# Kernel optimization log

Hardware: AMD Instinct MI355X
Metric: run time of the kernel (lower is better)

Reference implementation:

```python
import jax, jax.numpy as jnp
import numpy as np
from math import pi

N = 256        # in_features == out_features
BATCH = 131072


def givens_orthogonal(angles, n):
    """Build an n x n orthogonal matrix as the ordered product of Givens
    rotations G(i, j, theta_k) over pairs i < j in lexicographic order.
    Each rotation mixes rows i and j; applied sequentially via lax.scan."""
    ii, jj = np.triu_indices(n, 1)  # static pair order, len = n*(n-1)//2
    ii = jnp.asarray(ii, dtype=jnp.int32)
    jj = jnp.asarray(jj, dtype=jnp.int32)

    def body(M, t):
        i, j, th = t
        c, s = jnp.cos(th), jnp.sin(th)
        ri, rj = M[i], M[j]
        M = M.at[i].set(c * ri - s * rj)
        M = M.at[j].set(s * ri + c * rj)
        return M, None

    M0 = jnp.eye(n, dtype=angles.dtype)
    M, _ = jax.lax.scan(body, M0, (ii, jj, angles))
    return M


def setup_inputs() -> dict:
    key = jax.random.key(0)
    k1, k2, k3 = jax.random.split(key, 3)
    n_ang = N * (N - 1) // 2  # 32640
    return {
        "x": jax.random.normal(k1, (BATCH, N), dtype=jnp.float32),
        "Uweight": jax.random.uniform(k2, (n_ang,), minval=-pi / 2, maxval=pi / 2, dtype=jnp.float32),
        "Vweight": jax.random.uniform(k3, (n_ang,), minval=-pi / 2, maxval=pi / 2, dtype=jnp.float32),
        "Sweight": jnp.ones((N,), dtype=jnp.float32),
        "bias": jnp.zeros((N,), dtype=jnp.float32),
    }


def reference(x, Uweight, Vweight, Sweight, bias):
    # W = V @ diag(S) @ U^T  (SVD-parametrized weight, out x in)
    # y = x @ W^T + b = ((x @ U) * S) @ V^T + b   (square case in == out)
    U = givens_orthogonal(Uweight, N)  # (in, in) orthogonal
    V = givens_orthogonal(Vweight, N)  # (out, out) orthogonal
    return ((x @ U) * Sweight) @ V.T + bias
```

## Files before the change

### kernel.cpp

```cpp
#include <hip/hip_runtime.h>
#include <hip/hip_bf16.h>
#include <math.h>

#define NN 256
#define NPAIR 32640
#define NSEG 32
#define MAT (NN*NN)

#define MATS0 0
#define MATS1 (MATS0 + 64*MAT)
#define WBT_OFF (MATS1 + 32*MAT)

static __device__ const int BD[NSEG+1] =
    {0,4,8,12,16,20,24,28,32,37,42,47,52,57,62,67,73,79,85,91,97,
     104,111,118,126,134,143,153,164,177,192,213,255};
#define CSL_CAP 1120

typedef __attribute__((ext_vector_type(8))) short short8;
typedef __attribute__((ext_vector_type(4))) float f32x4;

__device__ __forceinline__ short f2bf(float f) {
    __hip_bfloat16 h = __float2bfloat16(f);
    return *reinterpret_cast<short*>(&h);
}

__global__ __launch_bounds__(64) void k_build(const float* __restrict__ au,
                                              const float* __restrict__ av,
                                              float* __restrict__ mats) {
    int b = blockIdx.x;
    int matid = b >> 7;
    int seg   = (b >> 2) & 31;
    int chunk = b & 3;
    int t = threadIdx.x;
    int c0 = chunk * 64;
    int i0 = BD[seg], i1 = BD[seg+1];
    float* outp = mats + (matid * NSEG + seg) * MAT;

    if (c0 + 64 <= i0) {
        for (int id = t; id < 4096; id += 64) {
            int row = id >> 4, c4 = (id & 15) * 4;
            float4 v = {0.f,0.f,0.f,0.f};
            int d = row - (c0 + c4);
            if (d >= 0 && d < 4) ((float*)&v)[d] = 1.0f;
            *(float4*)(outp + row*NN + c0 + c4) = v;
        }
        return;
    }

    __shared__ float M[NN * 64];
    __shared__ float2 csl[CSL_CAP];

    int kbase = 255*i0 - (i0*(i0-1))/2;
    int kend  = 255*i1 - (i1*(i1-1))/2;
    int nrot  = kend - kbase;
    const float* ang = (matid ? av : au) + kbase;
    for (int idx = t; idx < nrot; idx += 64) {
        float s, c;
        sincosf(ang[idx], &s, &c);
        float2 v = {c, s};
        csl[idx] = v;
    }

    int MR = NN - i0;
    for (int rr = 0; rr < MR; ++rr)
        M[rr*64 + t] = (i0 + rr == c0 + t) ? 1.0f : 0.0f;
    __syncthreads();

    for (int i = i0; i < i1; ++i) {
        int jstart = (i + 1 > c0) ? (i + 1) : c0;
        int kl = 255*i - (i*(i-1))/2 + (jstart - i - 1) - kbase;
        float ri = M[(i - i0)*64 + t];
        int j = jstart;
        int ng = (NN - jstart) >> 3;

        float2 cb[8]; float rj[8];
        if (ng > 0) {
#pragma unroll
            for (int u = 0; u < 8; ++u) cb[u] = csl[kl + u];
#pragma unroll
            for (int u = 0; u < 8; ++u) rj[u] = M[(j - i0 + u)*64 + t];
        }
        for (int g = 0; g < ng; ++g) {
            float2 cn[8]; float rn[8];
            if (g + 1 < ng) {
#pragma unroll
                for (int u = 0; u < 8; ++u) cn[u] = csl[kl + 8 + u];
#pragma unroll
                for (int u = 0; u < 8; ++u) rn[u] = M[(j + 8 - i0 + u)*64 + t];
            }
#pragma unroll
            for (int u = 0; u < 8; ++u) {
                float wv = cb[u].y*ri + cb[u].x*rj[u];
                ri       = cb[u].x*ri - cb[u].y*rj[u];
                M[(j - i0 + u)*64 + t] = wv;
            }
#pragma unroll
            for (int u = 0; u < 8; ++u) { cb[u] = cn[u]; rj[u] = rn[u]; }
            j += 8; kl += 8;
        }
        int rem = NN - j;
        if (rem > 0) {
            float2 cc[7]; float r7[7];
#pragma unroll
            for (int u = 0; u < 7; ++u)
                if (u < rem) { cc[u] = csl[kl + u];
                               r7[u] = M[(j - i0 + u)*64 + t]; }
#pragma unroll
            for (int u = 0; u < 7; ++u)
                if (u < rem) {
                    float wv = cc[u].y*ri + cc[u].x*r7[u];
                    ri       = cc[u].x*ri - cc[u].y*r7[u];
                    M[(j - i0 + u)*64 + t] = wv;
                }
        }
        M[(i - i0)*64 + t] = ri;
    }
    __syncthreads();

    for (int id = t; id < 4096; id += 64) {
        int row = id >> 4, c4 = (id & 15) * 4;
        float4 v;
        if (row < i0) {
            v = make_float4(0.f,0.f,0.f,0.f);
            int d = row - (c0 + c4);
            if (d >= 0 && d < 4) ((float*)&v)[d] = 1.0f;
        } else {
            v = *(const float4*)&M[(row - i0)*64 + c4];
        }
        *(float4*)(outp + row*NN + c0 + c4) = v;
    }
}

__global__ __launch_bounds__(256) void k_fold(const float* __restrict__ in,
                                              float* __restrict__ out,
                                              int nOut, int lg, int span) {
    int b = blockIdx.x;
    int np2 = 2 * nOut;
    int m    = b & (np2 - 1);
    int tile = b >> lg;
    int side = (m >= nOut) ? 1 : 0;
    int q = m - side * nOut;
    const float* A = in + (side*np2 + 2*q + 1) * MAT;
    const float* B = in + (side*np2 + 2*q) * MAT;
    float* C = out + m * MAT;
    int i0A = BD[q * span + (span >> 1)];
    int r0 = (tile >> 2) * 64, c0 = (tile & 3) * 64;
    int t = threadIdx.x;

    if (r0 + 64 <= i0A) {
#pragma unroll
        for (int u = 0; u < 4; ++u) {
            int id = u*256 + t;
            int rr = id >> 4, cc = (id & 15) * 4;
            *(float4*)(C + (r0+rr)*NN + c0 + cc) =
                *(const float4*)(B + (r0+rr)*NN + c0 + cc);
        }
        return;
    }

    int kstart = ((r0 < i0A) ? r0 : i0A) & ~31;
    int nt = (NN - kstart) >> 5;

    __shared__ float Ast[2][32][68];
    __shared__ float Bs [2][32][68];
    int tx = t & 15, ty = t >> 4;
    int arow = t >> 3, ak4 = t & 7;
    int bkr = t >> 4, bc4 = t & 15;

    float acc[4][4] = {};
    f32x4 pa0, pa1, pb0, pb1;
    {
        int kt = kstart;
        pa0 = *(const f32x4*)(A + (r0 + arow     )*NN + kt + ak4*4);
        pa1 = *(const f32x4*)(A + (r0 + arow + 32)*NN + kt + ak4*4);
        pb0 = *(const f32x4*)(B + (kt + bkr      )*NN + c0 + bc4*4);
        pb1 = *(const f32x4*)(B + (kt + bkr + 16 )*NN + c0 + bc4*4);
    }
    for (int it = 0; it < nt; ++it) {
        int cur = it & 1;
#pragma unroll
        for (int jj = 0; jj < 4; ++jj) {
            Ast[cur][ak4*4 + jj][arow]      = pa0[jj];
            Ast[cur][ak4*4 + jj][arow + 32] = pa1[jj];
        }
        *(f32x4*)&Bs[cur][bkr     ][bc4*4] = pb0;
        *(f32x4*)&Bs[cur][bkr + 16][bc4*4] = pb1;
        if (it + 1 < nt) {
            int k2 = kstart + (it+1)*32;
            pa0 = *(const f32x4*)(A + (r0 + arow     )*NN + k2 + ak4*4);
            pa1 = *(const f32x4*)(A + (r0 + arow + 32)*NN + k2 + ak4*4);
            pb0 = *(const f32x4*)(B + (k2 + bkr      )*NN + c0 + bc4*4);
            pb1 = *(const f32x4*)(B + (k2 + bkr + 16 )*NN + c0 + bc4*4);
        }
        __syncthreads();
#pragma unroll 8
        for (int kk = 0; kk < 32; ++kk) {
            f32x4 a4 = *(const f32x4*)&Ast[cur][kk][ty*4];
            f32x4 b4 = *(const f32x4*)&Bs [cur][kk][tx*4];
#pragma unroll
            for (int rr = 0; rr < 4; ++rr)
#pragma unroll
                for (int cc = 0; cc < 4; ++cc)
                    acc[rr][cc] = fmaf(a4[rr], b4[cc], acc[rr][cc]);
        }
    }
#pragma unroll
    for (int rr = 0; rr < 4; ++rr) {
        float4 o = {acc[rr][0], acc[rr][1], acc[rr][2], acc[rr][3]};
        *(float4*)(C + (r0 + ty*4 + rr)*NN + c0 + tx*4) = o;
    }
}

__global__ __launch_bounds__(256) void k_wmatT(const float* __restrict__ U,
                                               const float* __restrict__ V,
                                               const float* __restrict__ S,
                                               unsigned short* __restrict__ Wbt) {
    int b = blockIdx.x;
    int n0 = (b >> 4) * 16, i0 = (b & 15) * 16;
    int t = threadIdx.x, ti = t & 15, tn = t >> 4;
    __shared__ float Us[16][260];
    __shared__ float Vs[16][260];
    {
        int rr = t >> 4, cc = (t & 15) * 16;
#pragma unroll
        for (int q = 0; q < 4; ++q) {
            float4 u = *(const float4*)(U + (i0+rr)*NN + cc + q*4);
            float4 s = *(const float4*)(S + cc + q*4);
            u.x *= s.x; u.y *= s.y; u.z *= s.z; u.w *= s.w;
            *(float4*)&Us[rr][cc+q*4] = u;
            *(float4*)&Vs[rr][cc+q*4] = *(const float4*)(V + (n0+rr)*NN + cc + q*4);
        }
    }
    __syncthreads();
    float acc = 0.f;
#pragma unroll 8
    for (int k4 = 0; k4 < 64; ++k4) {
        float4 uu = *(const float4*)&Us[ti][k4*4];
        float4 vv = *(const float4*)&Vs[tn][k4*4];
        acc += uu.x*vv.x + uu.y*vv.y + uu.z*vv.z + uu.w*vv.w;
    }
    Wbt[(n0+tn)*NN + (i0+ti)] = (unsigned short)f2bf(acc);
}

__global__ __launch_bounds__(512, 4) void k_mm(const float* __restrict__ x,
                                               const unsigned short* __restrict__ Wbt,
                                               const float* __restrict__ bias,
                                               float* __restrict__ out) {
    int t = threadIdx.x;
    int w = t >> 6, l = t & 63, l15 = l & 15, lg = l >> 4;
    int n0 = w * 32;

    __shared__ unsigned short Xs[16 * 512];

    short8 bfrag[2][8];
#pragma unroll
    for (int nt = 0; nt < 2; ++nt) {
        const unsigned short* wrow = Wbt + (n0 + nt*16 + l15) * NN + lg * 8;
#pragma unroll
        for (int ks = 0; ks < 8; ++ks)
            bfrag[nt][ks] = *(const short8*)(wrow + ks * 32);
    }
    float b0 = bias[n0 + l15];
    float b1 = bias[n0 + 16 + l15];

    long row0 = (long)blockIdx.x * 32;
    int r = t & 15, m = t >> 4;
    int ksb = m >> 2;
    int lidx = r + 16 * (m & 3);
    const float* s0 = x + (row0 + r) * NN + 8*m;
    const float* s1 = s0 + 16 * NN;
    float4 a0 = *(const float4*)(s0);
    float4 a1 = *(const float4*)(s0 + 4);
    float4 c0 = *(const float4*)(s1);
    float4 c1 = *(const float4*)(s1 + 4);
    short8 h0, h1;
    h0[0]=f2bf(a0.x); h0[1]=f2bf(a0.y); h0[2]=f2bf(a0.z); h0[3]=f2bf(a0.w);
    h0[4]=f2bf(a1.x); h0[5]=f2bf(a1.y); h0[6]=f2bf(a1.z); h0[7]=f2bf(a1.w);
    h1[0]=f2bf(c0.x); h1[1]=f2bf(c0.y); h1[2]=f2bf(c0.z); h1[3]=f2bf(c0.w);
    h1[4]=f2bf(c1.x); h1[5]=f2bf(c1.y); h1[6]=f2bf(c1.z); h1[7]=f2bf(c1.w);
    *(short8*)&Xs[(0*8 + ksb)*512 + lidx*8] = h0;
    *(short8*)&Xs[(1*8 + ksb)*512 + lidx*8] = h1;
    __syncthreads();

#pragma unroll
    for (int tt = 0; tt < 2; ++tt) {
        f32x4 acc0 = {0.f,0.f,0.f,0.f}, acc1 = {0.f,0.f,0.f,0.f};
#pragma unroll
        for (int ks = 0; ks < 8; ++ks) {
            short8 af = *(const short8*)&Xs[(tt*8 + ks)*512 + l*8];
            acc0 = __builtin_amdgcn_mfma_f32_16x16x32_bf16(af, bfrag[0][ks], acc0, 0, 0, 0);
            acc1 = __builtin_amdgcn_mfma_f32_16x16x32_bf16(af, bfrag[1][ks], acc1, 0, 0, 0);
        }
        float* op = out + (row0 + tt*16 + lg*4) * NN + n0 + l15;
#pragma unroll
        for (int rr = 0; rr < 4; ++rr) {
            op[rr * NN]      = acc0[rr] + b0;
            op[rr * NN + 16] = acc1[rr] + b1;
        }
    }
}

extern "C" void kernel_launch(void* const* d_in, const int* in_sizes, int n_in,
                              void* d_out, int out_size, void* d_ws, size_t ws_size,
                              hipStream_t stream) {
    const float* x    = (const float*)d_in[0];
    const float* Uw   = (const float*)d_in[1];
    const float* Vw   = (const float*)d_in[2];
    const float* Sw   = (const float*)d_in[3];
    const float* bias = (const float*)d_in[4];
    float* out = (float*)d_out;
    float* ws  = (float*)d_ws;

    k_build<<<256, 64, 0, stream>>>(Uw, Vw, ws + MATS0);
    k_fold<<<16*32, 256, 0, stream>>>(ws + MATS0, ws + MATS1, 16, 5, 2);
    k_fold<<<16*16, 256, 0, stream>>>(ws + MATS1, ws + MATS0,  8, 4, 4);
    k_fold<<<16* 8, 256, 0, stream>>>(ws + MATS0, ws + MATS1,  4, 3, 8);
    k_fold<<<16* 4, 256, 0, stream>>>(ws + MATS1, ws + MATS0,  2, 2, 16);
    k_fold<<<16* 2, 256, 0, stream>>>(ws + MATS0, ws + MATS1,  1, 1, 32);
    k_wmatT<<<256, 256, 0, stream>>>(ws + MATS1, ws + MATS1 + MAT, Sw,
                                     (unsigned short*)(ws + WBT_OFF));
    k_mm<<<4096, 512, 0, stream>>>(x, (unsigned short*)(ws + WBT_OFF), bias, out);
}
```

Baseline: 227.6 us.

## Double-buffer x tiles in k_mm over 64 rows and relax fold barriers

The final GEMM kernel now has each block handle 64 rows instead of 32, in four 16-row steps. Each step converts the current x slice to bf16 into one of two LDS buffers while the next slice's global load is already in flight, so global latency overlaps with MFMA work. This halves the grid and the per-block reloading of the bf16 weight fragments and bias. A custom barrier that waits only on LDS counters replaces __syncthreads in the fold GEMM, so prefetched global loads are not drained at the barrier. The trade-off is fewer blocks, which may reduce latency hiding through occupancy.

```diff
diff --git a/kernel.cpp b/kernel.cpp
--- a/kernel.cpp
+++ b/kernel.cpp
@@ -23,6 +23,12 @@
     __hip_bfloat16 h = __float2bfloat16(f);
     return *reinterpret_cast<short*>(&h);
 }
+
+#define BAR() do {                                              \
+    asm volatile("s_waitcnt lgkmcnt(0)" ::: "memory");          \
+    __builtin_amdgcn_s_barrier();                               \
+    asm volatile("" ::: "memory");                              \
+} while (0)
 
 __global__ __launch_bounds__(64) void k_build(const float* __restrict__ au,
                                               const float* __restrict__ av,
@@ -192,7 +198,7 @@
             pb0 = *(const f32x4*)(B + (k2 + bkr      )*NN + c0 + bc4*4);
             pb1 = *(const f32x4*)(B + (k2 + bkr + 16 )*NN + c0 + bc4*4);
         }
-        __syncthreads();
+        BAR();
 #pragma unroll 8
         for (int kk = 0; kk < 32; ++kk) {
             f32x4 a4 = *(const f32x4*)&Ast[cur][kk][ty*4];
@@ -250,48 +256,50 @@
     int w = t >> 6, l = t & 63, l15 = l & 15, lg = l >> 4;
     int n0 = w * 32;
 
-    __shared__ unsigned short Xs[16 * 512];
-
-    short8 bfrag[2][8];
-#pragma unroll
-    for (int nt = 0; nt < 2; ++nt) {
-        const unsigned short* wrow = Wbt + (n0 + nt*16 + l15) * NN + lg * 8;
-#pragma unroll
-        for (int ks = 0; ks < 8; ++ks)
-            bfrag[nt][ks] = *(const short8*)(wrow + ks * 32);
-    }
-    float b0 = bias[n0 + l15];
-    float b1 = bias[n0 + 16 + l15];
-
-    long row0 = (long)blockIdx.x * 32;
+    __shared__ unsigned short Xs[2][8 * 512];
+
+    long row0 = (long)blockIdx.x * 64;
     int r = t & 15, m = t >> 4;
     int ksb = m >> 2;
     int lidx = r + 16 * (m & 3);
+
     const float* s0 = x + (row0 + r) * NN + 8*m;
-    const float* s1 = s0 + 16 * NN;
-    float4 a0 = *(const float4*)(s0);
-    float4 a1 = *(const float4*)(s0 + 4);
-    float4 c0 = *(const float4*)(s1);
-    float4 c1 = *(const float4*)(s1 + 4);
-    short8 h0, h1;
-    h0[0]=f2bf(a0.x); h0[1]=f2bf(a0.y); h0[2]=f2bf(a0.z); h0[3]=f2bf(a0.w);
-    h0[4]=f2bf(a1.x); h0[5]=f2bf(a1.y); h0[6]=f2bf(a1.z); h0[7]=f2bf(a1.w);
-    h1[0]=f2bf(c0.x); h1[1]=f2bf(c0.y); h1[2]=f2bf(c0.z); h1[3]=f2bf(c0.w);
-    h1[4]=f2bf(c1.x); h1[5]=f2bf(c1.y); h1[6]=f2bf(c1.z); h1[7]=f2bf(c1.w);
-    *(short8*)&Xs[(0*8 + ksb)*512 + lidx*8] = h0;
-    *(short8*)&Xs[(1*8 + ksb)*512 + lidx*8] = h1;
-    __syncthreads();
-
-#pragma unroll
-    for (int tt = 0; tt < 2; ++tt) {
+    float4 f0 = *(const float4*)(s0);
+    float4 f1 = *(const float4*)(s0 + 4);
+
+    short8 bfrag[2][8];
+#pragma unroll
+    for (int nt = 0; nt < 2; ++nt) {
+        const unsigned short* wrow = Wbt + (n0 + nt*16 + l15) * NN + lg * 8;
+#pragma unroll
+        for (int ks = 0; ks < 8; ++ks)
+            bfrag[nt][ks] = *(const short8*)(wrow + ks * 32);
+    }
+    float b0 = bias[n0 + l15];
+    float b1 = bias[n0 + 16 + l15];
+
+#pragma unroll
+    for (int it = 0; it < 4; ++it) {
+        int cur = it & 1;
+        short8 h;
+        h[0]=f2bf(f0.x); h[1]=f2bf(f0.y); h[2]=f2bf(f0.z); h[3]=f2bf(f0.w);
+        h[4]=f2bf(f1.x); h[5]=f2bf(f1.y); h[6]=f2bf(f1.z); h[7]=f2bf(f1.w);
+        *(short8*)&Xs[cur][ksb*512 + lidx*8] = h;
+        if (it < 3) {
+            const float* sn = x + (row0 + (it+1)*16 + r) * NN + 8*m;
+            f0 = *(const float4*)(sn);
+            f1 = *(const float4*)(sn + 4);
+        }
+        BAR();
+
         f32x4 acc0 = {0.f,0.f,0.f,0.f}, acc1 = {0.f,0.f,0.f,0.f};
 #pragma unroll
         for (int ks = 0; ks < 8; ++ks) {
-            short8 af = *(const short8*)&Xs[(tt*8 + ks)*512 + l*8];
+            short8 af = *(const short8*)&Xs[cur][ks*512 + l*8];
             acc0 = __builtin_amdgcn_mfma_f32_16x16x32_bf16(af, bfrag[0][ks], acc0, 0, 0, 0);
             acc1 = __builtin_amdgcn_mfma_f32_16x16x32_bf16(af, bfrag[1][ks], acc1, 0, 0, 0);
         }
-        float* op = out + (row0 + tt*16 + lg*4) * NN + n0 + l15;
+        float* op = out + (row0 + it*16 + lg*4) * NN + n0 + l15;
 #pragma unroll
         for (int rr = 0; rr < 4; ++rr) {
             op[rr * NN]      = acc0[rr] + b0;
@@ -319,5 +327,5 @@
     k_fold<<<16* 2, 256, 0, stream>>>(ws + MATS0, ws + MATS1,  1, 1, 32);
     k_wmatT<<<256, 256, 0, stream>>>(ws + MATS1, ws + MATS1 + MAT, Sw,
                                      (unsigned short*)(ws + WBT_OFF));
-    k_mm<<<4096, 512, 0, stream>>>(x, (unsigned short*)(ws + WBT_OFF), bias, out);
-}
+    k_mm<<<2048, 512, 0, stream>>>(x, (unsigned short*)(ws + WBT_OFF), bias, out);
+}
```

Result: faster. 215.8 us (-5.2%).
